# Kernel optimization log

Measured on AMD Instinct MI355X. Metric: run time of the kernel, lower is better.

The kernel has to match this reference:

```python
import jax, jax.numpy as jnp
import numpy as np

DIMS, HEAD, FREQ = 1024, 16, 10000
HEAD_DIM = DIMS // HEAD          # 64
ROT = HEAD_DIM // 2              # 32
B, S = 4, 8192


def setup_inputs() -> dict:
    key = jax.random.key(0)
    k1, k2, k3, k4 = jax.random.split(key, 4)
    x = jax.random.normal(k1, (B, S, DIMS), dtype=jnp.float32)
    matrix = jax.random.normal(k2, (HEAD_DIM, HEAD_DIM), dtype=jnp.float32)
    thetas = jax.random.normal(k3, (ROT,), dtype=jnp.float32) * 0.1
    tscale = jnp.ones((1,), dtype=jnp.float32)
    # inverse frequencies exactly as in __init__
    invf = (1.0 / FREQ ** (jnp.arange(0, HEAD_DIM, 2, dtype=jnp.float32) / HEAD_DIM)).astype(jnp.float32)
    pairs = jax.random.randint(k4, (ROT, 2), 0, HEAD_DIM, dtype=jnp.int32)
    return {"x": x, "matrix": matrix, "thetas": thetas, "tscale": tscale,
            "invf": invf, "pairs": pairs}


def _composed_rotation(thetas, tscale, pairs, d, dtype):
    # Build every Givens matrix G_k (same element-set order as the torch code)
    theta = thetas * tscale[0]

    def make_G(i, j, th):
        c, sn = jnp.cos(th), jnp.sin(th)
        G = jnp.eye(d, dtype=dtype)
        return G.at[i, i].set(c).at[j, j].set(c).at[i, j].set(-sn).at[j, i].set(sn)

    Gs = jax.vmap(make_G)(pairs[:, 0], pairs[:, 1], theta)  # [rot, d, d]

    def step(acc, G):
        return acc @ G, None

    G_comb, _ = jax.lax.scan(step, jnp.eye(d, dtype=dtype), Gs)
    return G_comb


def reference(x, matrix, thetas, tscale, invf, pairs):
    b, s, dims = x.shape
    d = matrix.shape[0]          # head_dim
    h = dims // d                # heads

    G_comb = _composed_rotation(thetas, tscale, pairs, d, x.dtype)

    xr = x.reshape(b, s, h, d)
    # flat @ G_combined @ self.matrix (acts on last dim)
    xr = xr @ (G_comb @ matrix)

    # sinusoidal RoPE: sinusoid[s, d/2] = pos * invf
    pos = jnp.arange(s, dtype=x.dtype)
    sinusoid = pos[:, None] * invf[None, :]
    sin = jnp.sin(sinusoid)[None, :, None, :]   # [1, s, 1, d/2]
    cos = jnp.cos(sinusoid)[None, :, None, :]

    x1, x2 = xr[..., ::2], xr[..., 1::2]
    out = jnp.concatenate([x1 * cos - x2 * sin, x1 * sin + x2 * cos], axis=-1)
    return out.reshape(b, s, dims) * jnp.asarray(np.sqrt(dims), x.dtype)
```

## Files before the change

### kernel.cpp

```cpp
#include <hip/hip_runtime.h>
#include <math.h>

#define BB 4
#define SS 8192
#define HH 16
#define DD 64
#define ROT 32
#define NG (BB * SS * HH)
#define RPB 128
#define LSTR 65

__global__ void setup_G(const float* __restrict__ thetas,
                        const float* __restrict__ tscale,
                        const int* __restrict__ pairs,
                        float* __restrict__ G) {
  __shared__ float Gs[DD][DD];
  const int t = threadIdx.x;
  for (int c = 0; c < DD; ++c) Gs[t][c] = (t == c) ? 1.0f : 0.0f;
  const float ts = tscale[0];
  for (int r = 0; r < ROT; ++r) {
    const int i = pairs[2 * r], j = pairs[2 * r + 1];
    const float th = thetas[r] * ts;
    const float cc = cosf(th), sn = sinf(th);
    if (i == j) {
      Gs[t][i] *= sn;
    } else {
      const float a = Gs[t][i], b = Gs[t][j];
      Gs[t][i] = a * cc + b * sn;
      Gs[t][j] = b * cc - a * sn;
    }
  }
  for (int c = 0; c < DD; ++c) G[t * DD + c] = Gs[t][c];
}

__global__ void setup_Mk(const float* __restrict__ G,
                         const float* __restrict__ matrix,
                         float* __restrict__ M) {
  const int e = blockIdx.x * 256 + threadIdx.x;
  const int row = e >> 6, col = e & 63;
  float a0 = 0.f, a1 = 0.f, a2 = 0.f, a3 = 0.f;
  for (int k = 0; k < DD; k += 4) {
    a0 = fmaf(G[row * DD + k], matrix[k * DD + col], a0);
    a1 = fmaf(G[row * DD + k + 1], matrix[(k + 1) * DD + col], a1);
    a2 = fmaf(G[row * DD + k + 2], matrix[(k + 2) * DD + col], a2);
    a3 = fmaf(G[row * DD + k + 3], matrix[(k + 3) * DD + col], a3);
  }
  M[e] = (a0 + a1) + (a2 + a3);
}

__global__ void setup_table(const float* __restrict__ invf,
                            float* __restrict__ tab) {
  const int idx = blockIdx.x * 256 + threadIdx.x;
  if (idx >= SS * 32) return;
  const int s = idx >> 5, d = idx & 31;
  const float ang = (float)s * invf[d];
  tab[s * 64 + d] = 32.0f * cosf(ang);
  tab[s * 64 + 32 + d] = 32.0f * sinf(ang);
}

__global__ __launch_bounds__(256) void apply_rot(
    const float* __restrict__ x, const float* __restrict__ M,
    const float* __restrict__ tab, const float* __restrict__ invf,
    float* __restrict__ out) {
  __shared__ float lds[RPB * LSTR];
  const int tid = threadIdx.x;
  const size_t R0 = (size_t)blockIdx.x * RPB;

  const float4* __restrict__ xg = (const float4*)x + R0 * 16;
#pragma unroll
  for (int i = 0; i < 8; ++i) {
    const int f = i * 256 + tid;
    const int row = f >> 4, c4 = f & 15;
    const float4 v = xg[f];
    *(float4*)&lds[row * LSTR + c4 * 4] = v;
  }
  __syncthreads();

  const int r = tid & (RPB - 1);
  const int h = __builtin_amdgcn_readfirstlane(tid >> 7);
  const float* __restrict__ Mh = M + h * 32;
  const float* __restrict__ xr = &lds[r * LSTR];

  float acc[32];
#pragma unroll
  for (int c = 0; c < 32; ++c) acc[c] = 0.0f;

  for (int k4 = 0; k4 < 16; ++k4) {
    const float4 xv = *(const float4*)&xr[k4 * 4];
    const float* __restrict__ m0 = Mh + k4 * 4 * DD;
#pragma unroll
    for (int c = 0; c < 32; ++c) acc[c] = fmaf(xv.x, m0[c], acc[c]);
#pragma unroll
    for (int c = 0; c < 32; ++c) acc[c] = fmaf(xv.y, m0[DD + c], acc[c]);
#pragma unroll
    for (int c = 0; c < 32; ++c) acc[c] = fmaf(xv.z, m0[2 * DD + c], acc[c]);
#pragma unroll
    for (int c = 0; c < 32; ++c) acc[c] = fmaf(xv.w, m0[3 * DD + c], acc[c]);
  }

  const int g = (int)R0 + r;
  const int spos = (g >> 4) & (SS - 1);
  float cz[16], sz[16];
  if (tab) {
    const float4* __restrict__ tc = (const float4*)(tab + spos * 64 + h * 16);
    const float4* __restrict__ tn =
        (const float4*)(tab + spos * 64 + 32 + h * 16);
#pragma unroll
    for (int q = 0; q < 4; ++q) {
      *(float4*)&cz[4 * q] = tc[q];
      *(float4*)&sz[4 * q] = tn[q];
    }
  } else {
#pragma unroll
    for (int d = 0; d < 16; ++d) {
      const float ang = (float)spos * invf[h * 16 + d];
      cz[d] = 32.0f * cosf(ang);
      sz[d] = 32.0f * sinf(ang);
    }
  }

  float lo[16], hi[16];
#pragma unroll
  for (int d = 0; d < 16; ++d) {
    const float e = acc[2 * d], o = acc[2 * d + 1];
    lo[d] = e * cz[d] - o * sz[d];
    hi[d] = e * sz[d] + o * cz[d];
  }

  __syncthreads();
  float* __restrict__ orow = &lds[r * LSTR];
#pragma unroll
  for (int q = 0; q < 4; ++q) {
    *(float4*)&orow[16 * h + 4 * q] = *(float4*)&lo[4 * q];
    *(float4*)&orow[32 + 16 * h + 4 * q] = *(float4*)&hi[4 * q];
  }
  __syncthreads();

  float4* __restrict__ og = (float4*)out + R0 * 16;
#pragma unroll
  for (int i = 0; i < 8; ++i) {
    const int f = i * 256 + tid;
    const int row = f >> 4, c4 = f & 15;
    og[f] = *(float4*)&lds[row * LSTR + c4 * 4];
  }
}

extern "C" void kernel_launch(void* const* d_in, const int* in_sizes, int n_in,
                              void* d_out, int out_size, void* d_ws,
                              size_t ws_size, hipStream_t stream) {
  const float* x = (const float*)d_in[0];
  const float* matrix = (const float*)d_in[1];
  const float* thetas = (const float*)d_in[2];
  const float* tscale = (const float*)d_in[3];
  const float* invf = (const float*)d_in[4];
  const int* pairs = (const int*)d_in[5];
  float* out = (float*)d_out;

  float* G = (float*)d_ws;
  float* M = G + DD * DD;
  float* tab = M + DD * DD;
  const size_t need = (size_t)(2 * DD * DD + SS * 64) * sizeof(float);
  const bool have_tab = ws_size >= need;

  setup_G<<<1, 64, 0, stream>>>(thetas, tscale, pairs, G);
  setup_Mk<<<16, 256, 0, stream>>>(G, matrix, M);
  if (have_tab) setup_table<<<(SS * 32) / 256, 256, 0, stream>>>(invf, tab);
  apply_rot<<<NG / RPB, 256, 0, stream>>>(x, M, have_tab ? tab : nullptr, invf,
                                          out);
}
```

Measured before the change: 285.6 us.

## Restructure rotation kernel into single-wave blocks with register-prefetched tiles

The main kernel now runs one 64-thread wave per block. Each block processes four 64-row tiles in turn, and each thread computes all 64 output columns of its row instead of splitting a row's columns across two waves. The next tile is loaded into registers while the current one is computed, so global loads overlap with the FMAs. The G and M setup kernels are merged into one launch. In exchange, each thread holds 64 accumulators plus 16 float4 prefetch registers, which raises register pressure and may lower occupancy. The block count drops, but barriers between LDS use and the global loads go away.

```diff
diff --git a/kernel.cpp b/kernel.cpp
--- a/kernel.cpp
+++ b/kernel.cpp
@@ -7,45 +7,41 @@
 #define DD 64
 #define ROT 32
 #define NG (BB * SS * HH)
-#define RPB 128
-#define LSTR 65
+#define TILES (NG / DD)
+#define TPB 4
+#define GRID (TILES / TPB)
+#define LSTR 68
 
-__global__ void setup_G(const float* __restrict__ thetas,
+__global__ void setup_M(const float* __restrict__ matrix,
+                        const float* __restrict__ thetas,
                         const float* __restrict__ tscale,
-                        const int* __restrict__ pairs,
-                        float* __restrict__ G) {
-  __shared__ float Gs[DD][DD];
+                        const int* __restrict__ pairs, float* __restrict__ M) {
+  __shared__ float G[DD * DD];
   const int t = threadIdx.x;
-  for (int c = 0; c < DD; ++c) Gs[t][c] = (t == c) ? 1.0f : 0.0f;
-  const float ts = tscale[0];
-  for (int r = 0; r < ROT; ++r) {
-    const int i = pairs[2 * r], j = pairs[2 * r + 1];
-    const float th = thetas[r] * ts;
-    const float cc = cosf(th), sn = sinf(th);
-    if (i == j) {
-      Gs[t][i] *= sn;
-    } else {
-      const float a = Gs[t][i], b = Gs[t][j];
-      Gs[t][i] = a * cc + b * sn;
-      Gs[t][j] = b * cc - a * sn;
+  for (int i = t; i < DD * DD; i += 256) G[i] = ((i / DD) == (i % DD)) ? 1.f : 0.f;
+  __syncthreads();
+  if (t < DD) {
+    const float ts = tscale[0];
+    for (int r = 0; r < ROT; ++r) {
+      const int i = pairs[2 * r], j = pairs[2 * r + 1];
+      const float th = thetas[r] * ts;
+      const float cc = cosf(th), sn = sinf(th);
+      if (i == j) {
+        G[t * DD + i] *= sn;
+      } else {
+        const float a = G[t * DD + i], b = G[t * DD + j];
+        G[t * DD + i] = a * cc + b * sn;
+        G[t * DD + j] = b * cc - a * sn;
+      }
     }
   }
-  for (int c = 0; c < DD; ++c) G[t * DD + c] = Gs[t][c];
-}
-
-__global__ void setup_Mk(const float* __restrict__ G,
-                         const float* __restrict__ matrix,
-                         float* __restrict__ M) {
-  const int e = blockIdx.x * 256 + threadIdx.x;
-  const int row = e >> 6, col = e & 63;
-  float a0 = 0.f, a1 = 0.f, a2 = 0.f, a3 = 0.f;
-  for (int k = 0; k < DD; k += 4) {
-    a0 = fmaf(G[row * DD + k], matrix[k * DD + col], a0);
-    a1 = fmaf(G[row * DD + k + 1], matrix[(k + 1) * DD + col], a1);
-    a2 = fmaf(G[row * DD + k + 2], matrix[(k + 2) * DD + col], a2);
-    a3 = fmaf(G[row * DD + k + 3], matrix[(k + 3) * DD + col], a3);
+  __syncthreads();
+  for (int e = t; e < DD * DD; e += 256) {
+    const int row = e >> 6, col = e & 63;
+    float s = 0.f;
+    for (int k = 0; k < DD; ++k) s = fmaf(G[row * DD + k], matrix[k * DD + col], s);
+    M[e] = s;
   }
-  M[e] = (a0 + a1) + (a2 + a3);
 }
 
 __global__ void setup_table(const float* __restrict__ invf,
@@ -58,90 +54,87 @@
   tab[s * 64 + 32 + d] = 32.0f * sinf(ang);
 }
 
-__global__ __launch_bounds__(256) void apply_rot(
+__global__ __launch_bounds__(64, 2) void apply_rot(
     const float* __restrict__ x, const float* __restrict__ M,
     const float* __restrict__ tab, const float* __restrict__ invf,
     float* __restrict__ out) {
-  __shared__ float lds[RPB * LSTR];
-  const int tid = threadIdx.x;
-  const size_t R0 = (size_t)blockIdx.x * RPB;
+  __shared__ float buf[DD * LSTR];
+  const int l = threadIdx.x;
+  const int tile0 = blockIdx.x * TPB;
+  const int rbase = l >> 4, c4 = l & 15;
 
-  const float4* __restrict__ xg = (const float4*)x + R0 * 16;
+  float4 st[16];
+  {
+    const float4* __restrict__ xg = (const float4*)x + (size_t)tile0 * DD * 16;
 #pragma unroll
-  for (int i = 0; i < 8; ++i) {
-    const int f = i * 256 + tid;
-    const int row = f >> 4, c4 = f & 15;
-    const float4 v = xg[f];
-    *(float4*)&lds[row * LSTR + c4 * 4] = v;
-  }
-  __syncthreads();
-
-  const int r = tid & (RPB - 1);
-  const int h = __builtin_amdgcn_readfirstlane(tid >> 7);
-  const float* __restrict__ Mh = M + h * 32;
-  const float* __restrict__ xr = &lds[r * LSTR];
-
-  float acc[32];
-#pragma unroll
-  for (int c = 0; c < 32; ++c) acc[c] = 0.0f;
-
-  for (int k4 = 0; k4 < 16; ++k4) {
-    const float4 xv = *(const float4*)&xr[k4 * 4];
-    const float* __restrict__ m0 = Mh + k4 * 4 * DD;
-#pragma unroll
-    for (int c = 0; c < 32; ++c) acc[c] = fmaf(xv.x, m0[c], acc[c]);
-#pragma unroll
-    for (int c = 0; c < 32; ++c) acc[c] = fmaf(xv.y, m0[DD + c], acc[c]);
-#pragma unroll
-    for (int c = 0; c < 32; ++c) acc[c] = fmaf(xv.z, m0[2 * DD + c], acc[c]);
-#pragma unroll
-    for (int c = 0; c < 32; ++c) acc[c] = fmaf(xv.w, m0[3 * DD + c], acc[c]);
+    for (int j = 0; j < 16; ++j) st[j] = xg[j * 64 + l];
   }
 
-  const int g = (int)R0 + r;
-  const int spos = (g >> 4) & (SS - 1);
-  float cz[16], sz[16];
-  if (tab) {
-    const float4* __restrict__ tc = (const float4*)(tab + spos * 64 + h * 16);
-    const float4* __restrict__ tn =
-        (const float4*)(tab + spos * 64 + 32 + h * 16);
+  for (int t = 0; t < TPB; ++t) {
+    const int tile = tile0 + t;
+
+#pragma unroll
+    for (int j = 0; j < 16; ++j)
+      *(float4*)&buf[(4 * j + rbase) * LSTR + c4 * 4] = st[j];
+
+    if (t + 1 < TPB) {
+      const float4* __restrict__ xg =
+          (const float4*)x + (size_t)(tile + 1) * DD * 16;
+#pragma unroll
+      for (int j = 0; j < 16; ++j) st[j] = xg[j * 64 + l];
+    }
+
+    float acc[DD];
+#pragma unroll
+    for (int c = 0; c < DD; ++c) acc[c] = 0.f;
+    const float* __restrict__ xr = &buf[l * LSTR];
+#pragma unroll
+    for (int k4 = 0; k4 < 16; ++k4) {
+      const float4 xv = *(const float4*)&xr[k4 * 4];
+      const float* __restrict__ m = M + k4 * 4 * DD;
+#pragma unroll
+      for (int c = 0; c < DD; ++c) acc[c] = fmaf(xv.x, m[c], acc[c]);
+#pragma unroll
+      for (int c = 0; c < DD; ++c) acc[c] = fmaf(xv.y, m[DD + c], acc[c]);
+#pragma unroll
+      for (int c = 0; c < DD; ++c) acc[c] = fmaf(xv.z, m[2 * DD + c], acc[c]);
+#pragma unroll
+      for (int c = 0; c < DD; ++c) acc[c] = fmaf(xv.w, m[3 * DD + c], acc[c]);
+    }
+
+    const int spos = (int)(((size_t)tile * DD + l) >> 4) & (SS - 1);
+    const float* __restrict__ tb = tab + (size_t)spos * 64;
+    float* __restrict__ orow = &buf[l * LSTR];
 #pragma unroll
     for (int q = 0; q < 4; ++q) {
-      *(float4*)&cz[4 * q] = tc[q];
-      *(float4*)&sz[4 * q] = tn[q];
+      float cz[8], sz[8];
+      if (tab) {
+#pragma unroll
+        for (int i = 0; i < 8; ++i) {
+          cz[i] = tb[8 * q + i];
+          sz[i] = tb[32 + 8 * q + i];
+        }
+      } else {
+#pragma unroll
+        for (int i = 0; i < 8; ++i) {
+          const float ang = (float)spos * invf[8 * q + i];
+          cz[i] = 32.0f * cosf(ang);
+          sz[i] = 32.0f * sinf(ang);
+        }
+      }
+#pragma unroll
+      for (int i = 0; i < 8; ++i) {
+        const int d = 8 * q + i;
+        const float e = acc[2 * d], o = acc[2 * d + 1];
+        orow[d] = e * cz[i] - o * sz[i];
+        orow[32 + d] = e * sz[i] + o * cz[i];
+      }
     }
-  } else {
+
+    float4* __restrict__ og = (float4*)out + (size_t)tile * DD * 16;
 #pragma unroll
-    for (int d = 0; d < 16; ++d) {
-      const float ang = (float)spos * invf[h * 16 + d];
-      cz[d] = 32.0f * cosf(ang);
-      sz[d] = 32.0f * sinf(ang);
-    }
-  }
-
-  float lo[16], hi[16];
-#pragma unroll
-  for (int d = 0; d < 16; ++d) {
-    const float e = acc[2 * d], o = acc[2 * d + 1];
-    lo[d] = e * cz[d] - o * sz[d];
-    hi[d] = e * sz[d] + o * cz[d];
-  }
-
-  __syncthreads();
-  float* __restrict__ orow = &lds[r * LSTR];
-#pragma unroll
-  for (int q = 0; q < 4; ++q) {
-    *(float4*)&orow[16 * h + 4 * q] = *(float4*)&lo[4 * q];
-    *(float4*)&orow[32 + 16 * h + 4 * q] = *(float4*)&hi[4 * q];
-  }
-  __syncthreads();
-
-  float4* __restrict__ og = (float4*)out + R0 * 16;
-#pragma unroll
-  for (int i = 0; i < 8; ++i) {
-    const int f = i * 256 + tid;
-    const int row = f >> 4, c4 = f & 15;
-    og[f] = *(float4*)&lds[row * LSTR + c4 * 4];
+    for (int j = 0; j < 16; ++j)
+      og[j * 64 + l] = *(const float4*)&buf[(4 * j + rbase) * LSTR + c4 * 4];
   }
 }
 
@@ -156,15 +149,12 @@
   const int* pairs = (const int*)d_in[5];
   float* out = (float*)d_out;
 
-  float* G = (float*)d_ws;
-  float* M = G + DD * DD;
+  float* M = (float*)d_ws;
   float* tab = M + DD * DD;
-  const size_t need = (size_t)(2 * DD * DD + SS * 64) * sizeof(float);
+  const size_t need = (size_t)(DD * DD + SS * 64) * sizeof(float);
   const bool have_tab = ws_size >= need;
 
-  setup_G<<<1, 64, 0, stream>>>(thetas, tscale, pairs, G);
-  setup_Mk<<<16, 256, 0, stream>>>(G, matrix, M);
+  setup_M<<<1, 256, 0, stream>>>(matrix, thetas, tscale, pairs, M);
   if (have_tab) setup_table<<<(SS * 32) / 256, 256, 0, stream>>>(invf, tab);
-  apply_rot<<<NG / RPB, 256, 0, stream>>>(x, M, have_tab ? tab : nullptr, invf,
-                                          out);
+  apply_rot<<<GRID, 64, 0, stream>>>(x, M, have_tab ? tab : nullptr, invf, out);
 }
```

After: 634.3 us. +122.1%, slower.
